# Performance work log

Hardware: AMD Instinct MI355X
Metric: run time of the kernel (lower is better)

The kernel has to match this reference:

```python
import jax, jax.numpy as jnp
import numpy as np

N = 100000      # num nodes
E = 1600000     # num edges (avg degree 16)
F_IN = 256      # num_node_features
HID = 128       # hid_dim
C = 16          # num_classes


def gcn_conv(x, W, b, src, dst, num_nodes):
    # Linear transform first (PyG GCNConv transforms then aggregates)
    h = x @ W  # [N, out]
    # Symmetric normalization with self-loops already included in src/dst
    ones = jnp.ones_like(dst, dtype=h.dtype)
    deg = jax.ops.segment_sum(ones, dst, num_segments=num_nodes)  # in-degree incl. self-loop
    dinv = jnp.where(deg > 0, jax.lax.rsqrt(deg), 0.0)
    norm = dinv[src] * dinv[dst]                 # [E+N]
    msg = h[src] * norm[:, None]                 # gather + scale
    out = jax.ops.segment_sum(msg, dst, num_segments=num_nodes)  # scatter-add
    return out + b


def setup_inputs() -> dict:
    key = jax.random.key(0)
    k = jax.random.split(key, 4)
    x = jax.random.normal(k[0], (N, F_IN), dtype=jnp.float32)
    edge_index = jax.random.randint(k[1], (2, E), 0, N, dtype=jnp.int32)
    W1 = jax.random.normal(k[2], (F_IN, HID), dtype=jnp.float32) * (1.0 / np.sqrt(F_IN))
    b1 = jnp.zeros((HID,), dtype=jnp.float32)
    W2 = jax.random.normal(k[3], (HID, C), dtype=jnp.float32) * (1.0 / np.sqrt(HID))
    b2 = jnp.zeros((C,), dtype=jnp.float32)
    return {"x": x, "edge_index": edge_index, "W1": W1, "b1": b1, "W2": W2, "b2": b2}


def reference(x, edge_index, W1, b1, W2, b2):
    num_nodes = x.shape[0]
    loop = jnp.arange(num_nodes, dtype=edge_index.dtype)
    src = jnp.concatenate([edge_index[0], loop])  # add self-loops
    dst = jnp.concatenate([edge_index[1], loop])
    h = gcn_conv(x, W1, b1, src, dst, num_nodes)
    h = jax.nn.relu(h)
    # F.dropout(training=self.training): identity in eval mode
    out = gcn_conv(h, W2, b2, src, dst, num_nodes)
    return out
```

## Files before the change

### kernel.cpp

```cpp
#include <hip/hip_runtime.h>
#include <cstddef>

#define CAP 48
#define NBUILD 4096

typedef short short8 __attribute__((ext_vector_type(8)));
typedef float floatx4 __attribute__((ext_vector_type(4)));

__device__ inline float b2f_lo(unsigned int u) {
  union { unsigned int i; float f; } c;
  c.i = u << 16;
  return c.f;
}
__device__ inline float b2f_hi(unsigned int u) {
  union { unsigned int i; float f; } c;
  c.i = u & 0xFFFF0000u;
  return c.f;
}
__device__ inline unsigned short f2b(float f) {
  union { float f; unsigned int i; } c;
  c.f = f;
  unsigned int u = c.i;
  unsigned int r = (u + 0x7FFFu + ((u >> 16) & 1u)) >> 16;
  return (unsigned short)r;
}
__device__ inline float dinv_of(int c) { return rsqrtf((float)(c + 1)); }

__global__ void k_prep(int* __restrict__ cnt, int N,
                       const float* __restrict__ W1, unsigned short* __restrict__ W1T) {
  int i = blockIdx.x * 256 + threadIdx.x;
  if (i < N) cnt[i] = 0;
  if (i < 256 * 128) {
    int k = i >> 7, n = i & 127;
    W1T[n * 256 + k] = f2b(W1[i]);
  }
}

__global__ __launch_bounds__(256) void k_build_gemm1(
    const int* __restrict__ src, const int* __restrict__ dst, int E, int N,
    int* __restrict__ cnt, int* __restrict__ bucket,
    const float* __restrict__ X, const unsigned short* __restrict__ W1T,
    unsigned short* __restrict__ H1, int M, int gblocks, int total) {
  __shared__ unsigned short As[64 * 40];
  __shared__ unsigned short Bs[128 * 40];

  const unsigned int idx = blockIdx.x;
  const unsigned int gBefore = (idx * (unsigned int)gblocks) / (unsigned int)total;
  const unsigned int gAfter = ((idx + 1) * (unsigned int)gblocks) / (unsigned int)total;
  const bool isGemm = (gAfter > gBefore);

  if (!isGemm) {
    const int bi = (int)(idx - gBefore);
    const int g = bi & 7;
    const int S = (N + 7) >> 3;
    const int lo = g * S;
    const int hi = min(N, lo + S);
    const int tb = (bi >> 3) * 256 + (int)threadIdx.x;
    const int T = (NBUILD >> 3) * 256;
    const int E4 = E & ~3;

    for (int i0 = tb * 4; i0 < E4; i0 += T * 4) {
      int4 d4 = *(const int4*)(dst + i0);
      int4 s4 = *(const int4*)(src + i0);
      int p0 = CAP, p1 = CAP, p2 = CAP, p3 = CAP;
      if (d4.x >= lo && d4.x < hi) p0 = atomicAdd(&cnt[d4.x], 1);
      if (d4.y >= lo && d4.y < hi) p1 = atomicAdd(&cnt[d4.y], 1);
      if (d4.z >= lo && d4.z < hi) p2 = atomicAdd(&cnt[d4.z], 1);
      if (d4.w >= lo && d4.w < hi) p3 = atomicAdd(&cnt[d4.w], 1);
      if (p0 < CAP) bucket[(size_t)d4.x * CAP + p0] = s4.x;
      if (p1 < CAP) bucket[(size_t)d4.y * CAP + p1] = s4.y;
      if (p2 < CAP) bucket[(size_t)d4.z * CAP + p2] = s4.z;
      if (p3 < CAP) bucket[(size_t)d4.w * CAP + p3] = s4.w;
    }
    if (tb < E - E4) {
      int i = E4 + tb;
      int d = dst[i], s = src[i];
      if (d >= lo && d < hi) {
        int pos = atomicAdd(&cnt[d], 1);
        if (pos < CAP) bucket[(size_t)d * CAP + pos] = s;
      }
    }
    return;
  }

  const int bid = (int)gBefore;
  const int tid = threadIdx.x;
  const int wave = tid >> 6;
  const int lane = tid & 63;
  const int quad = lane >> 4;
  const int l16 = lane & 15;
  const int row0 = bid * 64;
  const int n0 = wave * 32;

  floatx4 acc[4][2];
#pragma unroll
  for (int r = 0; r < 4; r++)
#pragma unroll
    for (int c = 0; c < 2; c++) acc[r][c] = (floatx4){0.f, 0.f, 0.f, 0.f};

  for (int k0 = 0; k0 < 256; k0 += 32) {
    {
      int r = tid >> 2;
      int q = tid & 3;
      int gr = row0 + r;
      float4 v0 = make_float4(0.f, 0.f, 0.f, 0.f), v1 = v0;
      if (gr < M) {
        const float4* xp = (const float4*)(X + (size_t)gr * 256 + k0 + q * 8);
        v0 = xp[0];
        v1 = xp[1];
      }
      unsigned short tmp[8];
      tmp[0] = f2b(v0.x); tmp[1] = f2b(v0.y); tmp[2] = f2b(v0.z); tmp[3] = f2b(v0.w);
      tmp[4] = f2b(v1.x); tmp[5] = f2b(v1.y); tmp[6] = f2b(v1.z); tmp[7] = f2b(v1.w);
      *(uint4*)(As + r * 40 + q * 8) = *(const uint4*)(tmp);
    }
    {
      int n = tid >> 1;
      int half = (tid & 1) * 16;
      const uint4* wp = (const uint4*)(W1T + (size_t)n * 256 + k0 + half);
      uint4 w0 = wp[0];
      uint4 w1 = wp[1];
      unsigned short* p = Bs + n * 40 + half;
      *(uint4*)(p) = w0;
      *(uint4*)(p + 8) = w1;
    }
    __syncthreads();

    short8 afr[4], bfr[2];
#pragma unroll
    for (int r = 0; r < 4; r++)
      afr[r] = *(const short8*)(As + (r * 16 + l16) * 40 + quad * 8);
#pragma unroll
    for (int c = 0; c < 2; c++)
      bfr[c] = *(const short8*)(Bs + (n0 + c * 16 + l16) * 40 + quad * 8);
#pragma unroll
    for (int r = 0; r < 4; r++)
#pragma unroll
      for (int c = 0; c < 2; c++)
        acc[r][c] = __builtin_amdgcn_mfma_f32_16x16x32_bf16(afr[r], bfr[c], acc[r][c], 0, 0, 0);
    __syncthreads();
  }

#pragma unroll
  for (int r = 0; r < 4; r++) {
#pragma unroll
    for (int c = 0; c < 2; c++) {
      int col = n0 + c * 16 + l16;
#pragma unroll
      for (int i = 0; i < 4; i++) {
        int gr = row0 + r * 16 + quad * 4 + i;
        if (gr < M) H1[(size_t)gr * 128 + col] = f2b(acc[r][c][i]);
      }
    }
  }
}

__global__ __launch_bounds__(256) void k_agg1(const unsigned short* __restrict__ H1,
                                              const int* __restrict__ cnt,
                                              const int* __restrict__ bucket,
                                              const float* __restrict__ b1,
                                              unsigned short* __restrict__ A1, int N) {
  const int lane = threadIdx.x & 15;
  const int node = blockIdx.x * 16 + (threadIdx.x >> 4);
  if (node >= N) return;
  const int cn = cnt[node];
  const float di = dinv_of(cn);
  const float wself = di * di;
  const int deg = min(cn, CAP);
  const int* bk = bucket + (size_t)node * CAP;

  int idx0 = (lane < deg) ? bk[lane] : 0;
  int idx1 = (lane + 16 < deg) ? bk[lane + 16] : 0;
  int idx2 = (lane + 32 < deg) ? bk[lane + 32] : 0;
  float dv0 = (lane < deg) ? dinv_of(cnt[idx0]) : 0.f;
  float dv1 = (lane + 16 < deg) ? dinv_of(cnt[idx1]) : 0.f;
  float dv2 = (lane + 32 < deg) ? dinv_of(cnt[idx2]) : 0.f;

  uint4 hs = ((const uint4*)(H1 + (size_t)node * 128))[lane];
  float a0 = b2f_lo(hs.x) * wself, a1 = b2f_hi(hs.x) * wself;
  float a2 = b2f_lo(hs.y) * wself, a3 = b2f_hi(hs.y) * wself;
  float a4 = b2f_lo(hs.z) * wself, a5 = b2f_hi(hs.z) * wself;
  float a6 = b2f_lo(hs.w) * wself, a7 = b2f_hi(hs.w) * wself;
  float c0 = 0.f, c1 = 0.f, c2 = 0.f, c3 = 0.f, c4 = 0.f, c5 = 0.f, c6 = 0.f, c7 = 0.f;

  for (int j = 0; j < deg; j += 4) {
    int b = j >> 4;
    int idxB = (b == 0) ? idx0 : ((b == 1) ? idx1 : idx2);
    float dvB = (b == 0) ? dv0 : ((b == 1) ? dv1 : dv2);
    int base = j & 15;
    int s0 = __shfl(idxB, base + 0, 16);
    int s1 = __shfl(idxB, base + 1, 16);
    int s2 = __shfl(idxB, base + 2, 16);
    int s3 = __shfl(idxB, base + 3, 16);
    float w0 = __shfl(dvB, base + 0, 16) * di;
    float w1 = __shfl(dvB, base + 1, 16) * di;
    float w2 = __shfl(dvB, base + 2, 16) * di;
    float w3 = __shfl(dvB, base + 3, 16) * di;
    uint4 v0 = ((const uint4*)(H1 + (size_t)s0 * 128))[lane];
    uint4 v1 = ((const uint4*)(H1 + (size_t)s1 * 128))[lane];
    uint4 v2 = ((const uint4*)(H1 + (size_t)s2 * 128))[lane];
    uint4 v3 = ((const uint4*)(H1 + (size_t)s3 * 128))[lane];
    a0 += b2f_lo(v0.x) * w0; a1 += b2f_hi(v0.x) * w0;
    a2 += b2f_lo(v0.y) * w0; a3 += b2f_hi(v0.y) * w0;
    a4 += b2f_lo(v0.z) * w0; a5 += b2f_hi(v0.z) * w0;
    a6 += b2f_lo(v0.w) * w0; a7 += b2f_hi(v0.w) * w0;
    c0 += b2f_lo(v1.x) * w1; c1 += b2f_hi(v1.x) * w1;
    c2 += b2f_lo(v1.y) * w1; c3 += b2f_hi(v1.y) * w1;
    c4 += b2f_lo(v1.z) * w1; c5 += b2f_hi(v1.z) * w1;
    c6 += b2f_lo(v1.w) * w1; c7 += b2f_hi(v1.w) * w1;
    a0 += b2f_lo(v2.x) * w2; a1 += b2f_hi(v2.x) * w2;
    a2 += b2f_lo(v2.y) * w2; a3 += b2f_hi(v2.y) * w2;
    a4 += b2f_lo(v2.z) * w2; a5 += b2f_hi(v2.z) * w2;
    a6 += b2f_lo(v2.w) * w2; a7 += b2f_hi(v2.w) * w2;
    c0 += b2f_lo(v3.x) * w3; c1 += b2f_hi(v3.x) * w3;
    c2 += b2f_lo(v3.y) * w3; c3 += b2f_hi(v3.y) * w3;
    c4 += b2f_lo(v3.z) * w3; c5 += b2f_hi(v3.z) * w3;
    c6 += b2f_lo(v3.w) * w3; c7 += b2f_hi(v3.w) * w3;
  }
  a0 += c0; a1 += c1; a2 += c2; a3 += c3;
  a4 += c4; a5 += c5; a6 += c6; a7 += c7;

  float4 bb0 = ((const float4*)b1)[lane * 2];
  float4 bb1 = ((const float4*)b1)[lane * 2 + 1];
  a0 = fmaxf(a0 + bb0.x, 0.f); a1 = fmaxf(a1 + bb0.y, 0.f);
  a2 = fmaxf(a2 + bb0.z, 0.f); a3 = fmaxf(a3 + bb0.w, 0.f);
  a4 = fmaxf(a4 + bb1.x, 0.f); a5 = fmaxf(a5 + bb1.y, 0.f);
  a6 = fmaxf(a6 + bb1.z, 0.f); a7 = fmaxf(a7 + bb1.w, 0.f);
  uint4 o;
  o.x = (unsigned int)f2b(a0) | ((unsigned int)f2b(a1) << 16);
  o.y = (unsigned int)f2b(a2) | ((unsigned int)f2b(a3) << 16);
  o.z = (unsigned int)f2b(a4) | ((unsigned int)f2b(a5) << 16);
  o.w = (unsigned int)f2b(a6) | ((unsigned int)f2b(a7) << 16);
  ((uint4*)(A1 + (size_t)node * 128))[lane] = o;
}

__global__ __launch_bounds__(256) void k_gemm2(const unsigned short* __restrict__ A1,
                                               const float* __restrict__ W2,
                                               unsigned short* __restrict__ H2, int M) {
  __shared__ float Ws[128 * 16];
  int tid = threadIdx.x;
  ((float4*)Ws)[tid] = ((const float4*)W2)[tid];
  ((float4*)Ws)[tid + 256] = ((const float4*)W2)[tid + 256];
  __syncthreads();
  int q = tid & 3;
  int row = blockIdx.x * 64 + (tid >> 2);
  if (row >= M) return;
  float4 acc = make_float4(0.f, 0.f, 0.f, 0.f);
  const unsigned short* arow = A1 + (size_t)row * 128;
  for (int k0 = 0; k0 < 128; k0 += 8) {
    uint4 av = *(const uint4*)(arow + k0);
    float a[8];
    a[0] = b2f_lo(av.x); a[1] = b2f_hi(av.x);
    a[2] = b2f_lo(av.y); a[3] = b2f_hi(av.y);
    a[4] = b2f_lo(av.z); a[5] = b2f_hi(av.z);
    a[6] = b2f_lo(av.w); a[7] = b2f_hi(av.w);
#pragma unroll
    for (int kk = 0; kk < 8; kk++) {
      float4 wv = *(const float4*)&Ws[(k0 + kk) * 16 + q * 4];
      acc.x += a[kk] * wv.x; acc.y += a[kk] * wv.y;
      acc.z += a[kk] * wv.z; acc.w += a[kk] * wv.w;
    }
  }
  ushort4 o;
  o.x = f2b(acc.x); o.y = f2b(acc.y); o.z = f2b(acc.z); o.w = f2b(acc.w);
  ((ushort4*)(H2 + (size_t)row * 16))[q] = o;
}

__global__ __launch_bounds__(256) void k_agg2(const unsigned short* __restrict__ H2,
                                              const int* __restrict__ cnt,
                                              const int* __restrict__ bucket,
                                              const float* __restrict__ b2,
                                              float* __restrict__ out, int N) {
  const int half = threadIdx.x & 1;
  const int node = blockIdx.x * 128 + (threadIdx.x >> 1);
  if (node >= N) return;
  const int cn = cnt[node];
  const float di = dinv_of(cn);
  const float wself = di * di;
  const int deg = min(cn, CAP);
  const int* bk = bucket + (size_t)node * CAP;

  uint4 h = ((const uint4*)(H2 + (size_t)node * 16))[half];
  float a0 = b2f_lo(h.x) * wself, a1 = b2f_hi(h.x) * wself;
  float a2 = b2f_lo(h.y) * wself, a3 = b2f_hi(h.y) * wself;
  float a4 = b2f_lo(h.z) * wself, a5 = b2f_hi(h.z) * wself;
  float a6 = b2f_lo(h.w) * wself, a7 = b2f_hi(h.w) * wself;

  for (int j = 0; j < deg; j += 4) {
    int4 s4 = *(const int4*)(bk + j);
    int s0 = s4.x;
    int s1 = (j + 1 < deg) ? s4.y : 0;
    int s2 = (j + 2 < deg) ? s4.z : 0;
    int s3 = (j + 3 < deg) ? s4.w : 0;
    float w0 = dinv_of(cnt[s0]) * di;
    float w1 = (j + 1 < deg) ? dinv_of(cnt[s1]) * di : 0.f;
    float w2 = (j + 2 < deg) ? dinv_of(cnt[s2]) * di : 0.f;
    float w3 = (j + 3 < deg) ? dinv_of(cnt[s3]) * di : 0.f;
    uint4 v0 = ((const uint4*)(H2 + (size_t)s0 * 16))[half];
    uint4 v1 = ((const uint4*)(H2 + (size_t)s1 * 16))[half];
    uint4 v2 = ((const uint4*)(H2 + (size_t)s2 * 16))[half];
    uint4 v3 = ((const uint4*)(H2 + (size_t)s3 * 16))[half];
    a0 += b2f_lo(v0.x) * w0 + b2f_lo(v1.x) * w1 + b2f_lo(v2.x) * w2 + b2f_lo(v3.x) * w3;
    a1 += b2f_hi(v0.x) * w0 + b2f_hi(v1.x) * w1 + b2f_hi(v2.x) * w2 + b2f_hi(v3.x) * w3;
    a2 += b2f_lo(v0.y) * w0 + b2f_lo(v1.y) * w1 + b2f_lo(v2.y) * w2 + b2f_lo(v3.y) * w3;
    a3 += b2f_hi(v0.y) * w0 + b2f_hi(v1.y) * w1 + b2f_hi(v2.y) * w2 + b2f_hi(v3.y) * w3;
    a4 += b2f_lo(v0.z) * w0 + b2f_lo(v1.z) * w1 + b2f_lo(v2.z) * w2 + b2f_lo(v3.z) * w3;
    a5 += b2f_hi(v0.z) * w0 + b2f_hi(v1.z) * w1 + b2f_hi(v2.z) * w2 + b2f_hi(v3.z) * w3;
    a6 += b2f_lo(v0.w) * w0 + b2f_lo(v1.w) * w1 + b2f_lo(v2.w) * w2 + b2f_lo(v3.w) * w3;
    a7 += b2f_hi(v0.w) * w0 + b2f_hi(v1.w) * w1 + b2f_hi(v2.w) * w2 + b2f_hi(v3.w) * w3;
  }

  float4 bb0 = ((const float4*)b2)[half * 2];
  float4 bb1 = ((const float4*)b2)[half * 2 + 1];
  float4 o0 = make_float4(a0 + bb0.x, a1 + bb0.y, a2 + bb0.z, a3 + bb0.w);
  float4 o1 = make_float4(a4 + bb1.x, a5 + bb1.y, a6 + bb1.z, a7 + bb1.w);
  ((float4*)(out + (size_t)node * 16))[half * 2] = o0;
  ((float4*)(out + (size_t)node * 16))[half * 2 + 1] = o1;
}


extern "C" void kernel_launch(void* const* d_in, const int* in_sizes, int n_in,
                              void* d_out, int out_size, void* d_ws, size_t ws_size,
                              hipStream_t stream) {
  const float* x  = (const float*)d_in[0];
  const int* eidx = (const int*)d_in[1];
  const float* W1 = (const float*)d_in[2];
  const float* b1 = (const float*)d_in[3];
  const float* W2 = (const float*)d_in[4];
  const float* b2 = (const float*)d_in[5];
  float* out = (float*)d_out;

  const int HID = in_sizes[3];
  const int F   = in_sizes[2] / HID;
  const int N   = in_sizes[0] / F;
  const int E   = in_sizes[1] / 2;
  (void)n_in; (void)out_size; (void)ws_size;

  const int* src = eidx;
  const int* dst = eidx + E;

  char* base = (char*)d_ws;
  size_t off = 0;
  auto alloc = [&](size_t bytes) -> char* {
    char* p = base + off;
    off = (off + bytes + 255) & ~(size_t)255;
    return p;
  };
  int*            cnt    = (int*)alloc((size_t)N * 4);
  int*            bucket = (int*)alloc((size_t)N * CAP * 4);
  unsigned short* w1t    = (unsigned short*)alloc((size_t)256 * 128 * 2);
  unsigned short* h1     = (unsigned short*)alloc((size_t)N * 128 * 2);
  unsigned short* a1     = (unsigned short*)alloc((size_t)N * 128 * 2);
  unsigned short* h2     = (unsigned short*)alloc((size_t)N * 16 * 2);

  const int nbN = (N + 255) / 256;
  const int gblocks = (N + 63) / 64;
  const int total = NBUILD + gblocks;

  hipLaunchKernelGGL(k_prep, dim3(nbN), dim3(256), 0, stream, cnt, N, W1, w1t);
  hipLaunchKernelGGL(k_build_gemm1, dim3(total), dim3(256), 0, stream,
                     src, dst, E, N, cnt, bucket, x, w1t, h1, N, gblocks, total);
  hipLaunchKernelGGL(k_agg1, dim3((N + 15) / 16), dim3(256), 0, stream, h1, cnt, bucket,
                     b1, a1, N);
  hipLaunchKernelGGL(k_gemm2, dim3((N + 63) / 64), dim3(256), 0, stream, a1, W2, h2, N);
  hipLaunchKernelGGL(k_agg2, dim3((N + 127) / 128), dim3(256), 0, stream, h2, cnt, bucket,
                     b2, out, N);
}
```

Measured before the change: 338.6 us.

## Fuse layer-1 aggregation with layer-2 GEMM and use nontemporal loads/stores

Merges the layer-1 aggregation kernel with the small 128x16 second GEMM. Each 16-lane group multiplies its 8 ReLU'd features by W2 held in shared memory, then reduces the partial sums with a butterfly of xor shuffles so each lane ends with one output column. This removes the round trip of the N x 128 bf16 intermediate A1 through global memory and one kernel launch. It also switches the X loads and H1 stores in GEMM1 to nontemporal hints and folds the v3 accumulation into the a-accumulators. The costs are extra per-node shuffles and shared-memory reads, and reduced ILP in the gather loop from the accumulator change.

```diff
diff --git a/kernel.cpp b/kernel.cpp
--- a/kernel.cpp
+++ b/kernel.cpp
@@ -103,15 +103,15 @@
       int r = tid >> 2;
       int q = tid & 3;
       int gr = row0 + r;
-      float4 v0 = make_float4(0.f, 0.f, 0.f, 0.f), v1 = v0;
+      floatx4 v0 = (floatx4){0.f, 0.f, 0.f, 0.f}, v1 = v0;
       if (gr < M) {
-        const float4* xp = (const float4*)(X + (size_t)gr * 256 + k0 + q * 8);
-        v0 = xp[0];
-        v1 = xp[1];
+        const floatx4* xp = (const floatx4*)(X + (size_t)gr * 256 + k0 + q * 8);
+        v0 = __builtin_nontemporal_load(xp);
+        v1 = __builtin_nontemporal_load(xp + 1);
       }
       unsigned short tmp[8];
-      tmp[0] = f2b(v0.x); tmp[1] = f2b(v0.y); tmp[2] = f2b(v0.z); tmp[3] = f2b(v0.w);
-      tmp[4] = f2b(v1.x); tmp[5] = f2b(v1.y); tmp[6] = f2b(v1.z); tmp[7] = f2b(v1.w);
+      tmp[0] = f2b(v0[0]); tmp[1] = f2b(v0[1]); tmp[2] = f2b(v0[2]); tmp[3] = f2b(v0[3]);
+      tmp[4] = f2b(v1[0]); tmp[5] = f2b(v1[1]); tmp[6] = f2b(v1[2]); tmp[7] = f2b(v1[3]);
       *(uint4*)(As + r * 40 + q * 8) = *(const uint4*)(tmp);
     }
     {
@@ -149,17 +149,27 @@
 #pragma unroll
       for (int i = 0; i < 4; i++) {
         int gr = row0 + r * 16 + quad * 4 + i;
-        if (gr < M) H1[(size_t)gr * 128 + col] = f2b(acc[r][c][i]);
+        if (gr < M)
+          __builtin_nontemporal_store(f2b(acc[r][c][i]), &H1[(size_t)gr * 128 + col]);
       }
     }
   }
 }
 
-__global__ __launch_bounds__(256) void k_agg1(const unsigned short* __restrict__ H1,
-                                              const int* __restrict__ cnt,
-                                              const int* __restrict__ bucket,
-                                              const float* __restrict__ b1,
-                                              unsigned short* __restrict__ A1, int N) {
+__global__ __launch_bounds__(256) void k_agg1g2(const unsigned short* __restrict__ H1,
+                                                const int* __restrict__ cnt,
+                                                const int* __restrict__ bucket,
+                                                const float* __restrict__ b1,
+                                                const float* __restrict__ W2,
+                                                unsigned short* __restrict__ H2, int N) {
+  __shared__ float Ws[128 * 16];
+  {
+    int tid = threadIdx.x;
+    ((float4*)Ws)[tid] = ((const float4*)W2)[tid];
+    ((float4*)Ws)[tid + 256] = ((const float4*)W2)[tid + 256];
+  }
+  __syncthreads();
+
   const int lane = threadIdx.x & 15;
   const int node = blockIdx.x * 16 + (threadIdx.x >> 4);
   if (node >= N) return;
@@ -212,58 +222,76 @@
     a2 += b2f_lo(v2.y) * w2; a3 += b2f_hi(v2.y) * w2;
     a4 += b2f_lo(v2.z) * w2; a5 += b2f_hi(v2.z) * w2;
     a6 += b2f_lo(v2.w) * w2; a7 += b2f_hi(v2.w) * w2;
-    c0 += b2f_lo(v3.x) * w3; c1 += b2f_hi(v3.x) * w3;
-    c2 += b2f_lo(v3.y) * w3; c3 += b2f_hi(v3.y) * w3;
-    c4 += b2f_lo(v3.z) * w3; c5 += b2f_hi(v3.z) * w3;
-    c6 += b2f_lo(v3.w) * w3; c7 += b2f_hi(v3.w) * w3;
+    a0 += b2f_lo(v3.x) * w3; a1 += b2f_hi(v3.x) * w3;
+    a2 += b2f_lo(v3.y) * w3; a3 += b2f_hi(v3.y) * w3;
+    a4 += b2f_lo(v3.z) * w3; a5 += b2f_hi(v3.z) * w3;
+    a6 += b2f_lo(v3.w) * w3; a7 += b2f_hi(v3.w) * w3;
   }
   a0 += c0; a1 += c1; a2 += c2; a3 += c3;
   a4 += c4; a5 += c5; a6 += c6; a7 += c7;
 
   float4 bb0 = ((const float4*)b1)[lane * 2];
   float4 bb1 = ((const float4*)b1)[lane * 2 + 1];
-  a0 = fmaxf(a0 + bb0.x, 0.f); a1 = fmaxf(a1 + bb0.y, 0.f);
-  a2 = fmaxf(a2 + bb0.z, 0.f); a3 = fmaxf(a3 + bb0.w, 0.f);
-  a4 = fmaxf(a4 + bb1.x, 0.f); a5 = fmaxf(a5 + bb1.y, 0.f);
-  a6 = fmaxf(a6 + bb1.z, 0.f); a7 = fmaxf(a7 + bb1.w, 0.f);
-  uint4 o;
-  o.x = (unsigned int)f2b(a0) | ((unsigned int)f2b(a1) << 16);
-  o.y = (unsigned int)f2b(a2) | ((unsigned int)f2b(a3) << 16);
-  o.z = (unsigned int)f2b(a4) | ((unsigned int)f2b(a5) << 16);
-  o.w = (unsigned int)f2b(a6) | ((unsigned int)f2b(a7) << 16);
-  ((uint4*)(A1 + (size_t)node * 128))[lane] = o;
-}
-
-__global__ __launch_bounds__(256) void k_gemm2(const unsigned short* __restrict__ A1,
-                                               const float* __restrict__ W2,
-                                               unsigned short* __restrict__ H2, int M) {
-  __shared__ float Ws[128 * 16];
-  int tid = threadIdx.x;
-  ((float4*)Ws)[tid] = ((const float4*)W2)[tid];
-  ((float4*)Ws)[tid + 256] = ((const float4*)W2)[tid + 256];
-  __syncthreads();
-  int q = tid & 3;
-  int row = blockIdx.x * 64 + (tid >> 2);
-  if (row >= M) return;
-  float4 acc = make_float4(0.f, 0.f, 0.f, 0.f);
-  const unsigned short* arow = A1 + (size_t)row * 128;
-  for (int k0 = 0; k0 < 128; k0 += 8) {
-    uint4 av = *(const uint4*)(arow + k0);
-    float a[8];
-    a[0] = b2f_lo(av.x); a[1] = b2f_hi(av.x);
-    a[2] = b2f_lo(av.y); a[3] = b2f_hi(av.y);
-    a[4] = b2f_lo(av.z); a[5] = b2f_hi(av.z);
-    a[6] = b2f_lo(av.w); a[7] = b2f_hi(av.w);
-#pragma unroll
-    for (int kk = 0; kk < 8; kk++) {
-      float4 wv = *(const float4*)&Ws[(k0 + kk) * 16 + q * 4];
-      acc.x += a[kk] * wv.x; acc.y += a[kk] * wv.y;
-      acc.z += a[kk] * wv.z; acc.w += a[kk] * wv.w;
-    }
-  }
-  ushort4 o;
-  o.x = f2b(acc.x); o.y = f2b(acc.y); o.z = f2b(acc.z); o.w = f2b(acc.w);
-  ((ushort4*)(H2 + (size_t)row * 16))[q] = o;
+  float av[8];
+  av[0] = fmaxf(a0 + bb0.x, 0.f); av[1] = fmaxf(a1 + bb0.y, 0.f);
+  av[2] = fmaxf(a2 + bb0.z, 0.f); av[3] = fmaxf(a3 + bb0.w, 0.f);
+  av[4] = fmaxf(a4 + bb1.x, 0.f); av[5] = fmaxf(a5 + bb1.y, 0.f);
+  av[6] = fmaxf(a6 + bb1.z, 0.f); av[7] = fmaxf(a7 + bb1.w, 0.f);
+
+  float p[16];
+#pragma unroll
+  for (int c = 0; c < 16; c++) p[c] = 0.f;
+#pragma unroll
+  for (int i = 0; i < 8; i++) {
+    const float a = av[i];
+    const float* w = Ws + (lane * 8 + i) * 16;
+#pragma unroll
+    for (int c4 = 0; c4 < 4; c4++) {
+      float4 wv = *(const float4*)(w + c4 * 4);
+      p[c4 * 4 + 0] += a * wv.x;
+      p[c4 * 4 + 1] += a * wv.y;
+      p[c4 * 4 + 2] += a * wv.z;
+      p[c4 * 4 + 3] += a * wv.w;
+    }
+  }
+  float k8[8];
+  {
+    const bool hi = (lane & 8) != 0;
+#pragma unroll
+    for (int i = 0; i < 8; i++) {
+      float keep = hi ? p[8 + i] : p[i];
+      float send = hi ? p[i] : p[8 + i];
+      k8[i] = keep + __shfl_xor(send, 8, 16);
+    }
+  }
+  float k4[4];
+  {
+    const bool hi = (lane & 4) != 0;
+#pragma unroll
+    for (int i = 0; i < 4; i++) {
+      float keep = hi ? k8[4 + i] : k8[i];
+      float send = hi ? k8[i] : k8[4 + i];
+      k4[i] = keep + __shfl_xor(send, 4, 16);
+    }
+  }
+  float k2[2];
+  {
+    const bool hi = (lane & 2) != 0;
+#pragma unroll
+    for (int i = 0; i < 2; i++) {
+      float keep = hi ? k4[2 + i] : k4[i];
+      float send = hi ? k4[i] : k4[2 + i];
+      k2[i] = keep + __shfl_xor(send, 2, 16);
+    }
+  }
+  float v;
+  {
+    const bool hi = (lane & 1) != 0;
+    float keep = hi ? k2[1] : k2[0];
+    float send = hi ? k2[0] : k2[1];
+    v = keep + __shfl_xor(send, 1, 16);
+  }
+  H2[(size_t)node * 16 + lane] = f2b(v);
 }
 
 __global__ __launch_bounds__(256) void k_agg2(const unsigned short* __restrict__ H2,
@@ -350,7 +378,6 @@
   int*            bucket = (int*)alloc((size_t)N * CAP * 4);
   unsigned short* w1t    = (unsigned short*)alloc((size_t)256 * 128 * 2);
   unsigned short* h1     = (unsigned short*)alloc((size_t)N * 128 * 2);
-  unsigned short* a1     = (unsigned short*)alloc((size_t)N * 128 * 2);
   unsigned short* h2     = (unsigned short*)alloc((size_t)N * 16 * 2);
 
   const int nbN = (N + 255) / 256;
@@ -360,9 +387,8 @@
   hipLaunchKernelGGL(k_prep, dim3(nbN), dim3(256), 0, stream, cnt, N, W1, w1t);
   hipLaunchKernelGGL(k_build_gemm1, dim3(total), dim3(256), 0, stream,
                      src, dst, E, N, cnt, bucket, x, w1t, h1, N, gblocks, total);
-  hipLaunchKernelGGL(k_agg1, dim3((N + 15) / 16), dim3(256), 0, stream, h1, cnt, bucket,
-                     b1, a1, N);
-  hipLaunchKernelGGL(k_gemm2, dim3((N + 63) / 64), dim3(256), 0, stream, a1, W2, h2, N);
+  hipLaunchKernelGGL(k_agg1g2, dim3((N + 15) / 16), dim3(256), 0, stream, h1, cnt, bucket,
+                     b1, W2, h2, N);
   hipLaunchKernelGGL(k_agg2, dim3((N + 127) / 128), dim3(256), 0, stream, h2, cnt, bucket,
                      b2, out, N);
 }
```

New measurement: 386.5 us. 14.2% more time.
